# Kernel optimization log

Hardware: AMD Instinct MI355X
Metric: run time of the kernel (lower is better)

## Reference

```python
import jax, jax.numpy as jnp
import numpy as np

K = 4096      # kmer_num = 4^k with k=6
C = 10        # class_num
D = 128       # embedding dim
B = 1000      # batch of reads
L = 512       # kmers per read


def setup_inputs() -> dict:
    key = jax.random.key(0)
    k1, k2, k3, k4, k5 = jax.random.split(key, 5)
    u = jax.random.uniform(k1, (K, K))
    pair_counts = jnp.where(u > 0.9, jnp.floor(u * 50.0), 0.0).astype(jnp.float32)
    pair_counts = pair_counts * (1.0 - jnp.eye(K, dtype=jnp.float32))
    reads = jax.random.randint(k2, (B, L), 0, K, dtype=jnp.int32)
    read_labels = jax.random.randint(k3, (B,), 0, C, dtype=jnp.int32)
    embs = 2.0 * jax.random.uniform(k4, (K, D), dtype=jnp.float32) - 1.0
    softmax_weights = 2.0 * jax.random.uniform(k5, (C, D), dtype=jnp.float32) - 1.0
    delta = jnp.float32(0.5)
    return {"pair_counts": pair_counts, "reads": reads, "read_labels": read_labels,
            "delta": delta, "embs": embs, "softmax_weights": softmax_weights}


def reference(pair_counts, reads, read_labels, delta, embs, softmax_weights):
    # ---- supervised term: per-read bincount -> weighted emb sum -> log_softmax ----
    # counts[b, kmer] = number of occurrences of kmer in read b (batched bincount)
    counts = jnp.zeros((B, K), dtype=jnp.float32).at[
        jnp.arange(B)[:, None], reads].add(1.0)
    read_emb = counts @ embs                              # [B, D]
    logits = read_emb @ softmax_weights.T                 # [B, C]
    logp = jax.nn.log_softmax(logits, axis=1)             # [B, C]
    supervised = -jnp.sum(logp[jnp.arange(B), read_labels])

    # ---- unsupervised term: pairwise embedding distances over nonzero pairs ----
    sqn = jnp.sum(embs * embs, axis=1)                    # [K]
    sq = sqn[:, None] + sqn[None, :] - 2.0 * (embs @ embs.T)
    sq = jnp.maximum(sq, 0.0)                             # [K, K]
    mask = pair_counts != 0
    dist = jnp.sqrt(jnp.where(mask, sq, 1.0))             # safe sqrt off-edges
    rate = jnp.exp(-dist)
    # degrees * log(rate) - rate, with log(rate) = -dist, summed over nonzero pairs
    term = jnp.where(mask, -pair_counts * dist - rate, 0.0)
    scale = 1.0 / (np.float32(K) * np.float32(K))         # 1 / 4^(2k)
    unsupervised = -jnp.sum(term) * scale

    return delta * supervised + (1.0 - delta) * unsupervised
```

## Files before the change

### kernel.cpp

```cpp
#include <hip/hip_runtime.h>
#include <hip/hip_bf16.h>

#define KN 4096
#define CN 10
#define DN 128
#define BN 1000
#define LN 512

typedef float f32x4 __attribute__((ext_vector_type(4)));
typedef short bf16x8 __attribute__((ext_vector_type(8)));

__device__ __forceinline__ short bf16bits(float x) {
    __hip_bfloat16 h = __float2bfloat16(x);
    return *reinterpret_cast<short*>(&h);
}

__device__ __forceinline__ void gload_lds16(const float* g, float* l) {
    __builtin_amdgcn_global_load_lds(
        (const __attribute__((address_space(1))) void*)g,
        (__attribute__((address_space(3))) void*)l, 16, 0, 0);
}

__global__ __launch_bounds__(256) void w2v_prep(const float* __restrict__ embs,
                                                const float* __restrict__ W,
                                                float* __restrict__ sqn,
                                                short* __restrict__ ebf,
                                                float* __restrict__ P) {
    int blk = blockIdx.x, t = threadIdx.x;
    if (blk < 512) {
        int row = t >> 5, lane = t & 31;
        int r = blk * 8 + row;
        float4 v = ((const float4*)embs)[r * 32 + lane];
        short4 s4;
        s4.x = bf16bits(v.x); s4.y = bf16bits(v.y);
        s4.z = bf16bits(v.z); s4.w = bf16bits(v.w);
        ((short4*)ebf)[r * 32 + lane] = s4;
        float ss = v.x * v.x + v.y * v.y + v.z * v.z + v.w * v.w;
        #pragma unroll
        for (int m = 16; m >= 1; m >>= 1) ss += __shfl_xor(ss, m, 64);
        if (lane == 0) sqn[r] = ss;
        return;
    }
    int pb = blk - 512;
    int r = pb * 64 + (t >> 2);
    int q = t & 3;
    const float4* er = (const float4*)(embs + (size_t)r * DN) + q * 8;
    const float4* w4 = (const float4*)W;
    float s[CN];
    #pragma unroll
    for (int c = 0; c < CN; ++c) s[c] = 0.f;
    #pragma unroll
    for (int d4 = 0; d4 < 8; ++d4) {
        float4 e = er[d4];
        #pragma unroll
        for (int c = 0; c < CN; ++c) {
            float4 w = w4[c * 32 + q * 8 + d4];
            s[c] += e.x * w.x + e.y * w.y + e.z * w.z + e.w * w.w;
        }
    }
    #pragma unroll
    for (int c = 0; c < CN; ++c) {
        s[c] += __shfl_xor(s[c], 1, 64);
        s[c] += __shfl_xor(s[c], 2, 64);
    }
    if (q == 0) {
        float* pr = P + (size_t)r * 12;
        #pragma unroll
        for (int c = 0; c < CN; ++c) pr[c] = s[c];
        pr[10] = 0.f; pr[11] = 0.f;
    }
}

struct UnsupSm {
    float pcT[128 * 128];
    float sqi[128];
    float sqj[128];
    float wred[4];
};
struct SupSm {
    int   sidx[LN];
    float wredS[4][12];
    float slog[CN];
};
union K2Sm { UnsupSm u; SupSm s; };

__global__ __launch_bounds__(256, 2) void w2v_main(const short* __restrict__ ebf,
                                                   const float* __restrict__ sqn,
                                                   const float* __restrict__ pc,
                                                   const float* __restrict__ P,
                                                   const int* __restrict__ reads,
                                                   const int* __restrict__ labels,
                                                   float* __restrict__ psup,
                                                   float* __restrict__ puns) {
    __shared__ K2Sm sm;
    int blk = blockIdx.x, t = threadIdx.x;

    if (blk < 1024) {
        int i0 = (blk >> 5) * 128, j0 = (blk & 31) * 128;
        int wave = t >> 6, lane = t & 63;
        int wr = (wave >> 1) * 64, wc = (wave & 1) * 64;
        int lr = lane & 15, lg = lane >> 4;

        if (t < 128) sm.u.sqi[t] = sqn[i0 + t];
        else         sm.u.sqj[t - 128] = sqn[j0 + t - 128];

        const short* Ai = ebf + (size_t)(i0 + wr + lr) * DN;
        const short* Bj = ebf + (size_t)(j0 + wc + lr) * DN;
        bf16x8 afr[4][4], bfr[4][4];
        #pragma unroll
        for (int kk = 0; kk < 4; ++kk) {
            int ko = kk * 32 + lg * 8;
            #pragma unroll
            for (int mi = 0; mi < 4; ++mi) {
                afr[kk][mi] = *(const bf16x8*)(Ai + (size_t)mi * 16 * DN + ko);
                bfr[kk][mi] = *(const bf16x8*)(Bj + (size_t)mi * 16 * DN + ko);
            }
        }
        __builtin_amdgcn_sched_barrier(0);

        int rsub = lane >> 5, csub = lane & 31;
        #pragma unroll
        for (int c = 0; c < 16; ++c) {
            int row = wave * 32 + c * 2;
            const float* src = pc + (size_t)(i0 + row + rsub) * KN + j0 + csub * 4;
            gload_lds16(src, sm.u.pcT + row * 128);
        }

        f32x4 acc4[4][4];
        #pragma unroll
        for (int mi = 0; mi < 4; ++mi)
            #pragma unroll
            for (int nj = 0; nj < 4; ++nj)
                acc4[mi][nj] = (f32x4){0.f, 0.f, 0.f, 0.f};
        #pragma unroll
        for (int kk = 0; kk < 4; ++kk)
            #pragma unroll
            for (int mi = 0; mi < 4; ++mi)
                #pragma unroll
                for (int nj = 0; nj < 4; ++nj)
                    acc4[mi][nj] = __builtin_amdgcn_mfma_f32_16x16x32_bf16(
                        afr[kk][mi], bfr[kk][nj], acc4[mi][nj], 0, 0, 0);

        __syncthreads();

        float sj0 = sm.u.sqj[wc + lr],      sj1 = sm.u.sqj[wc + 16 + lr];
        float sj2 = sm.u.sqj[wc + 32 + lr], sj3 = sm.u.sqj[wc + 48 + lr];
        float part = 0.f;
        #pragma unroll
        for (int mi = 0; mi < 4; ++mi) {
            #pragma unroll
            for (int v = 0; v < 4; ++v) {
                int row = wr + 16 * mi + lg * 4 + v;
                float si = sm.u.sqi[row];
                const float* prow = sm.u.pcT + row * 128 + wc + lr;
                float p0 = prow[0], p1 = prow[16], p2 = prow[32], p3 = prow[48];
                float sq0 = fmaxf(si + sj0 - 2.f * acc4[mi][0][v], 0.f);
                float sq1 = fmaxf(si + sj1 - 2.f * acc4[mi][1][v], 0.f);
                float sq2 = fmaxf(si + sj2 - 2.f * acc4[mi][2][v], 0.f);
                float sq3 = fmaxf(si + sj3 - 2.f * acc4[mi][3][v], 0.f);
                float d0 = sqrtf(sq0), d1 = sqrtf(sq1);
                float d2 = sqrtf(sq2), d3 = sqrtf(sq3);
                float t0 = fmaf(p0, d0, __expf(-d0));
                float t1 = fmaf(p1, d1, __expf(-d1));
                float t2 = fmaf(p2, d2, __expf(-d2));
                float t3 = fmaf(p3, d3, __expf(-d3));
                part += (p0 != 0.f) ? t0 : 0.f;
                part += (p1 != 0.f) ? t1 : 0.f;
                part += (p2 != 0.f) ? t2 : 0.f;
                part += (p3 != 0.f) ? t3 : 0.f;
            }
        }
        #pragma unroll
        for (int off = 32; off > 0; off >>= 1) part += __shfl_down(part, off, 64);
        if (lane == 0) sm.u.wred[wave] = part;
        __syncthreads();
        if (t == 0)
            puns[blk] = (sm.u.wred[0] + sm.u.wred[1]) + (sm.u.wred[2] + sm.u.wred[3]);
        return;
    }

    int b = blk - 1024;
    for (int i = t; i < LN; i += 256) sm.s.sidx[i] = reads[b * LN + i];
    __syncthreads();
    const float4* P4 = (const float4*)P;
    size_t o0 = (size_t)sm.s.sidx[t] * 3;
    size_t o1 = (size_t)sm.s.sidx[t + 256] * 3;
    float4 a0 = P4[o0], b0 = P4[o0 + 1], c0 = P4[o0 + 2];
    float4 a1 = P4[o1], b1 = P4[o1 + 1], c1 = P4[o1 + 2];
    float s[12] = { a0.x + a1.x, a0.y + a1.y, a0.z + a1.z, a0.w + a1.w,
                    b0.x + b1.x, b0.y + b1.y, b0.z + b1.z, b0.w + b1.w,
                    c0.x + c1.x, c0.y + c1.y, c0.z + c1.z, c0.w + c1.w };
    #pragma unroll
    for (int off = 32; off > 0; off >>= 1)
        #pragma unroll
        for (int i = 0; i < 12; ++i) s[i] += __shfl_down(s[i], off, 64);
    int lane = t & 63, wave = t >> 6;
    if (lane == 0)
        #pragma unroll
        for (int i = 0; i < 12; ++i) sm.s.wredS[wave][i] = s[i];
    __syncthreads();
    if (t < CN)
        sm.s.slog[t] = sm.s.wredS[0][t] + sm.s.wredS[1][t]
                     + sm.s.wredS[2][t] + sm.s.wredS[3][t];
    __syncthreads();
    if (t == 0) {
        float m = sm.s.slog[0];
        #pragma unroll
        for (int c = 1; c < CN; ++c) m = fmaxf(m, sm.s.slog[c]);
        float se = 0.f;
        #pragma unroll
        for (int c = 0; c < CN; ++c) se += __expf(sm.s.slog[c] - m);
        float lse = m + __logf(se);
        psup[b] = -(sm.s.slog[labels[b]] - lse);
    }
}

__global__ __launch_bounds__(256) void w2v_final(const float* __restrict__ psup,
                                                 const float* __restrict__ puns,
                                                 const float* __restrict__ delta,
                                                 float* __restrict__ out) {
    __shared__ float r1[4], r2[4];
    int t = threadIdx.x;
    float a = 0.f, bsum = 0.f;
    for (int i = t; i < BN; i += 256)   a += psup[i];
    for (int i = t; i < 1024; i += 256) bsum += puns[i];
    #pragma unroll
    for (int off = 32; off > 0; off >>= 1) {
        a += __shfl_down(a, off, 64);
        bsum += __shfl_down(bsum, off, 64);
    }
    int lane = t & 63, wave = t >> 6;
    if (lane == 0) { r1[wave] = a; r2[wave] = bsum; }
    __syncthreads();
    if (t == 0) {
        float sup = (r1[0] + r1[1]) + (r1[2] + r1[3]);
        float uns = ((r2[0] + r2[1]) + (r2[2] + r2[3])) * (1.f / 16777216.f);
        float d = delta[0];
        out[0] = d * sup + (1.f - d) * uns;
    }
}

extern "C" void kernel_launch(void* const* d_in, const int* in_sizes, int n_in,
                              void* d_out, int out_size, void* d_ws, size_t ws_size,
                              hipStream_t stream) {
    const float* pc     = (const float*)d_in[0];
    const int*   reads  = (const int*)  d_in[1];
    const int*   labels = (const int*)  d_in[2];
    const float* delta  = (const float*)d_in[3];
    const float* embs   = (const float*)d_in[4];
    const float* W      = (const float*)d_in[5];
    float* out = (float*)d_out;

    char* ws = (char*)d_ws;
    float* sqn  = (float*)ws;
    float* P    = (float*)(ws + 16384);
    short* ebf  = (short*)(ws + 212992);
    float* psup = (float*)(ws + 1261568);
    float* puns = (float*)(ws + 1265664);

    w2v_prep<<<576, 256, 0, stream>>>(embs, W, sqn, ebf, P);
    w2v_main<<<2024, 256, 0, stream>>>(ebf, sqn, pc, P, reads, labels, psup, puns);
    w2v_final<<<1, 256, 0, stream>>>(psup, puns, delta, out);
}
```

Before: 55.50 us.

## Split main kernel into single-wave blocks with 32x128 tiles and no block barriers

Each block of the fused main kernel is now a single 64-thread wave. An unsupervised block covers a 32x128 tile, giving 4096 tiles, and a supervised block handles one read with a wave-only reduction. All __syncthreads are removed, and the pair-count tile is staged into padded LDS through async global-to-LDS loads. Split s_waitcnt points let the first half of the tile be processed while the second half is still in flight. The intent is better latency hiding and occupancy, at the cost of more blocks, more partial sums for the final reduction, and less reuse of the embedding rows per block.

```diff
diff --git a/kernel.cpp b/kernel.cpp
--- a/kernel.cpp
+++ b/kernel.cpp
@@ -6,6 +6,7 @@
 #define DN 128
 #define BN 1000
 #define LN 512
+#define UB 4096
 
 typedef float f32x4 __attribute__((ext_vector_type(4)));
 typedef short bf16x8 __attribute__((ext_vector_type(8)));
@@ -14,8 +15,7 @@
     __hip_bfloat16 h = __float2bfloat16(x);
     return *reinterpret_cast<short*>(&h);
 }
-
-__device__ __forceinline__ void gload_lds16(const float* g, float* l) {
+__device__ __forceinline__ void gload_lds16(const float* g, void* l) {
     __builtin_amdgcn_global_load_lds(
         (const __attribute__((address_space(1))) void*)g,
         (__attribute__((address_space(3))) void*)l, 16, 0, 0);
@@ -71,147 +71,126 @@
     }
 }
 
-struct UnsupSm {
-    float pcT[128 * 128];
-    float sqi[128];
-    float sqj[128];
-    float wred[4];
-};
-struct SupSm {
-    int   sidx[LN];
-    float wredS[4][12];
-    float slog[CN];
-};
-union K2Sm { UnsupSm u; SupSm s; };
-
-__global__ __launch_bounds__(256, 2) void w2v_main(const short* __restrict__ ebf,
-                                                   const float* __restrict__ sqn,
-                                                   const float* __restrict__ pc,
-                                                   const float* __restrict__ P,
-                                                   const int* __restrict__ reads,
-                                                   const int* __restrict__ labels,
-                                                   float* __restrict__ psup,
-                                                   float* __restrict__ puns) {
-    __shared__ K2Sm sm;
+__global__ __launch_bounds__(64) void w2v_main(const short* __restrict__ ebf,
+                                               const float* __restrict__ sqn,
+                                               const float* __restrict__ pc,
+                                               const float* __restrict__ P,
+                                               const int* __restrict__ reads,
+                                               const int* __restrict__ labels,
+                                               float* __restrict__ psup,
+                                               float* __restrict__ puns) {
+    __shared__ char pcT[16 * 1040];
     int blk = blockIdx.x, t = threadIdx.x;
 
-    if (blk < 1024) {
-        int i0 = (blk >> 5) * 128, j0 = (blk & 31) * 128;
-        int wave = t >> 6, lane = t & 63;
-        int wr = (wave >> 1) * 64, wc = (wave & 1) * 64;
-        int lr = lane & 15, lg = lane >> 4;
-
-        if (t < 128) sm.u.sqi[t] = sqn[i0 + t];
-        else         sm.u.sqj[t - 128] = sqn[j0 + t - 128];
-
-        const short* Ai = ebf + (size_t)(i0 + wr + lr) * DN;
-        const short* Bj = ebf + (size_t)(j0 + wc + lr) * DN;
-        bf16x8 afr[4][4], bfr[4][4];
+    if (blk < UB) {
+        int i0 = (blk >> 5) * 32;
+        int j0 = (blk & 31) * 128;
+        int lr = t & 15, lg = t >> 4;
+
+        const short* Arow = ebf + (size_t)(i0 + lr) * DN;
+        const short* Brow = ebf + (size_t)(j0 + lr) * DN;
+
+        f32x4 acc4[2][8];
+        #pragma unroll
+        for (int mi = 0; mi < 2; ++mi)
+            #pragma unroll
+            for (int nj = 0; nj < 8; ++nj)
+                acc4[mi][nj] = (f32x4){0.f, 0.f, 0.f, 0.f};
+
         #pragma unroll
         for (int kk = 0; kk < 4; ++kk) {
             int ko = kk * 32 + lg * 8;
-            #pragma unroll
-            for (int mi = 0; mi < 4; ++mi) {
-                afr[kk][mi] = *(const bf16x8*)(Ai + (size_t)mi * 16 * DN + ko);
-                bfr[kk][mi] = *(const bf16x8*)(Bj + (size_t)mi * 16 * DN + ko);
+            bf16x8 a0 = *(const bf16x8*)(Arow + ko);
+            bf16x8 a1 = *(const bf16x8*)(Arow + (size_t)16 * DN + ko);
+            bf16x8 bfr[8];
+            #pragma unroll
+            for (int nj = 0; nj < 8; ++nj)
+                bfr[nj] = *(const bf16x8*)(Brow + (size_t)nj * 16 * DN + ko);
+            #pragma unroll
+            for (int nj = 0; nj < 8; ++nj) {
+                acc4[0][nj] = __builtin_amdgcn_mfma_f32_16x16x32_bf16(
+                    a0, bfr[nj], acc4[0][nj], 0, 0, 0);
+                acc4[1][nj] = __builtin_amdgcn_mfma_f32_16x16x32_bf16(
+                    a1, bfr[nj], acc4[1][nj], 0, 0, 0);
             }
         }
         __builtin_amdgcn_sched_barrier(0);
 
-        int rsub = lane >> 5, csub = lane & 31;
-        #pragma unroll
-        for (int c = 0; c < 16; ++c) {
-            int row = wave * 32 + c * 2;
-            const float* src = pc + (size_t)(i0 + row + rsub) * KN + j0 + csub * 4;
-            gload_lds16(src, sm.u.pcT + row * 128);
-        }
-
-        f32x4 acc4[4][4];
-        #pragma unroll
-        for (int mi = 0; mi < 4; ++mi)
-            #pragma unroll
-            for (int nj = 0; nj < 4; ++nj)
-                acc4[mi][nj] = (f32x4){0.f, 0.f, 0.f, 0.f};
-        #pragma unroll
-        for (int kk = 0; kk < 4; ++kk)
-            #pragma unroll
-            for (int mi = 0; mi < 4; ++mi)
+        float siv[8], sjv[8];
+        #pragma unroll
+        for (int mi = 0; mi < 2; ++mi)
+            #pragma unroll
+            for (int v = 0; v < 4; ++v)
+                siv[mi * 4 + v] = sqn[i0 + mi * 16 + lg * 4 + v];
+        #pragma unroll
+        for (int nj = 0; nj < 8; ++nj) sjv[nj] = sqn[j0 + nj * 16 + lr];
+        __builtin_amdgcn_sched_barrier(0);
+
+        int rsub = t >> 5, csub = t & 31;
+        #pragma unroll
+        for (int p = 0; p < 16; ++p) {
+            const float* src = pc + (size_t)(i0 + 2 * p + rsub) * KN + j0 + csub * 4;
+            gload_lds16(src, pcT + p * 1040);
+        }
+        __builtin_amdgcn_sched_barrier(0);
+
+        float part = 0.f;
+        #pragma unroll
+        for (int mi = 0; mi < 2; ++mi) {
+            if (mi == 0) { asm volatile("s_waitcnt vmcnt(8)" ::: "memory"); }
+            else         { asm volatile("s_waitcnt vmcnt(0)" ::: "memory"); }
+            __builtin_amdgcn_sched_barrier(0);
+            #pragma unroll
+            for (int v = 0; v < 4; ++v) {
+                int row = mi * 16 + lg * 4 + v;
+                const float* prow =
+                    (const float*)(pcT + (row >> 1) * 1040 + (row & 1) * 512);
+                float si = siv[mi * 4 + v];
                 #pragma unroll
-                for (int nj = 0; nj < 4; ++nj)
-                    acc4[mi][nj] = __builtin_amdgcn_mfma_f32_16x16x32_bf16(
-                        afr[kk][mi], bfr[kk][nj], acc4[mi][nj], 0, 0, 0);
-
-        __syncthreads();
-
-        float sj0 = sm.u.sqj[wc + lr],      sj1 = sm.u.sqj[wc + 16 + lr];
-        float sj2 = sm.u.sqj[wc + 32 + lr], sj3 = sm.u.sqj[wc + 48 + lr];
-        float part = 0.f;
-        #pragma unroll
-        for (int mi = 0; mi < 4; ++mi) {
-            #pragma unroll
-            for (int v = 0; v < 4; ++v) {
-                int row = wr + 16 * mi + lg * 4 + v;
-                float si = sm.u.sqi[row];
-                const float* prow = sm.u.pcT + row * 128 + wc + lr;
-                float p0 = prow[0], p1 = prow[16], p2 = prow[32], p3 = prow[48];
-                float sq0 = fmaxf(si + sj0 - 2.f * acc4[mi][0][v], 0.f);
-                float sq1 = fmaxf(si + sj1 - 2.f * acc4[mi][1][v], 0.f);
-                float sq2 = fmaxf(si + sj2 - 2.f * acc4[mi][2][v], 0.f);
-                float sq3 = fmaxf(si + sj3 - 2.f * acc4[mi][3][v], 0.f);
-                float d0 = sqrtf(sq0), d1 = sqrtf(sq1);
-                float d2 = sqrtf(sq2), d3 = sqrtf(sq3);
-                float t0 = fmaf(p0, d0, __expf(-d0));
-                float t1 = fmaf(p1, d1, __expf(-d1));
-                float t2 = fmaf(p2, d2, __expf(-d2));
-                float t3 = fmaf(p3, d3, __expf(-d3));
-                part += (p0 != 0.f) ? t0 : 0.f;
-                part += (p1 != 0.f) ? t1 : 0.f;
-                part += (p2 != 0.f) ? t2 : 0.f;
-                part += (p3 != 0.f) ? t3 : 0.f;
+                for (int nj = 0; nj < 8; ++nj) {
+                    float pp = prow[nj * 16 + lr];
+                    float sq = fmaxf(si + sjv[nj] - 2.f * acc4[mi][nj][v], 0.f);
+                    float dd = sqrtf(sq);
+                    float tt = fmaf(pp, dd, __expf(-dd));
+                    part += (pp != 0.f) ? tt : 0.f;
+                }
             }
         }
         #pragma unroll
         for (int off = 32; off > 0; off >>= 1) part += __shfl_down(part, off, 64);
-        if (lane == 0) sm.u.wred[wave] = part;
-        __syncthreads();
-        if (t == 0)
-            puns[blk] = (sm.u.wred[0] + sm.u.wred[1]) + (sm.u.wred[2] + sm.u.wred[3]);
+        if (t == 0) puns[blk] = part;
         return;
     }
 
-    int b = blk - 1024;
-    for (int i = t; i < LN; i += 256) sm.s.sidx[i] = reads[b * LN + i];
-    __syncthreads();
+    int b = blk - UB;
+    const int4* rr = (const int4*)(reads + (size_t)b * LN);
+    int4 r0 = rr[t * 2], r1 = rr[t * 2 + 1];
+    int idx[8] = { r0.x, r0.y, r0.z, r0.w, r1.x, r1.y, r1.z, r1.w };
     const float4* P4 = (const float4*)P;
-    size_t o0 = (size_t)sm.s.sidx[t] * 3;
-    size_t o1 = (size_t)sm.s.sidx[t + 256] * 3;
-    float4 a0 = P4[o0], b0 = P4[o0 + 1], c0 = P4[o0 + 2];
-    float4 a1 = P4[o1], b1 = P4[o1 + 1], c1 = P4[o1 + 2];
-    float s[12] = { a0.x + a1.x, a0.y + a1.y, a0.z + a1.z, a0.w + a1.w,
-                    b0.x + b1.x, b0.y + b1.y, b0.z + b1.z, b0.w + b1.w,
-                    c0.x + c1.x, c0.y + c1.y, c0.z + c1.z, c0.w + c1.w };
+    float s[12];
+    #pragma unroll
+    for (int i = 0; i < 12; ++i) s[i] = 0.f;
+    #pragma unroll
+    for (int k = 0; k < 8; ++k) {
+        size_t o = (size_t)idx[k] * 3;
+        float4 x = P4[o], y = P4[o + 1], z = P4[o + 2];
+        s[0] += x.x; s[1] += x.y; s[2]  += x.z; s[3]  += x.w;
+        s[4] += y.x; s[5] += y.y; s[6]  += y.z; s[7]  += y.w;
+        s[8] += z.x; s[9] += z.y; s[10] += z.z; s[11] += z.w;
+    }
     #pragma unroll
     for (int off = 32; off > 0; off >>= 1)
         #pragma unroll
-        for (int i = 0; i < 12; ++i) s[i] += __shfl_down(s[i], off, 64);
-    int lane = t & 63, wave = t >> 6;
-    if (lane == 0)
-        #pragma unroll
-        for (int i = 0; i < 12; ++i) sm.s.wredS[wave][i] = s[i];
-    __syncthreads();
-    if (t < CN)
-        sm.s.slog[t] = sm.s.wredS[0][t] + sm.s.wredS[1][t]
-                     + sm.s.wredS[2][t] + sm.s.wredS[3][t];
-    __syncthreads();
+        for (int i = 0; i < CN; ++i) s[i] += __shfl_down(s[i], off, 64);
     if (t == 0) {
-        float m = sm.s.slog[0];
-        #pragma unroll
-        for (int c = 1; c < CN; ++c) m = fmaxf(m, sm.s.slog[c]);
+        float m = s[0];
+        #pragma unroll
+        for (int c = 1; c < CN; ++c) m = fmaxf(m, s[c]);
         float se = 0.f;
         #pragma unroll
-        for (int c = 0; c < CN; ++c) se += __expf(sm.s.slog[c] - m);
+        for (int c = 0; c < CN; ++c) se += __expf(s[c] - m);
         float lse = m + __logf(se);
-        psup[b] = -(sm.s.slog[labels[b]] - lse);
+        psup[b] = -(s[labels[b]] - lse);
     }
 }
 
@@ -223,7 +202,7 @@
     int t = threadIdx.x;
     float a = 0.f, bsum = 0.f;
     for (int i = t; i < BN; i += 256)   a += psup[i];
-    for (int i = t; i < 1024; i += 256) bsum += puns[i];
+    for (int i = t; i < UB; i += 256)   bsum += puns[i];
     #pragma unroll
     for (int off = 32; off > 0; off >>= 1) {
         a += __shfl_down(a, off, 64);
@@ -259,6 +238,6 @@
     float* puns = (float*)(ws + 1265664);
 
     w2v_prep<<<576, 256, 0, stream>>>(embs, W, sqn, ebf, P);
-    w2v_main<<<2024, 256, 0, stream>>>(ebf, sqn, pc, P, reads, labels, psup, puns);
+    w2v_main<<<UB + BN, 64, 0, stream>>>(ebf, sqn, pc, P, reads, labels, psup, puns);
     w2v_final<<<1, 256, 0, stream>>>(psup, puns, delta, out);
 }
```

Measured after the change: 56.08 us. No clear change (+1.0%).
